# Kernel optimization log

Hardware: AMD Instinct MI355X
Metric: run time of the kernel (lower is better)

The kernel has to match this reference:

```python
import jax, jax.numpy as jnp
import numpy as np

U, I, NG, D, G, B = 100000, 50000, 20000, 64, 20, 16384
H_GE = (D + 2 * D) // 2  # 96, group_encoder hidden

def setup_inputs() -> dict:
    key = jax.random.key(0)
    ks = jax.random.split(key, 24)
    s = 0.1
    return {
        'group_inputs': jax.random.randint(ks[0], (B,), 0, NG),
        'item_inputs': jax.random.randint(ks[1], (B,), 0, I),
        'group_members': jax.random.randint(ks[2], (NG, G), 0, U),
        'eps': jax.random.normal(ks[3], (B, D), dtype=jnp.float32),
        'user_emb': jax.random.normal(ks[4], (U, D), dtype=jnp.float32) * s,
        'item_emb': jax.random.normal(ks[5], (I, D), dtype=jnp.float32) * s,
        # user_encoder: MLP(D, D, 1) -> Linear(D,D), ReLU, Linear(D,D)
        'ue_w1': jax.random.normal(ks[6], (D, D), dtype=jnp.float32) * s,
        'ue_b1': jnp.zeros((D,), jnp.float32),
        'ue_w2': jax.random.normal(ks[7], (D, D), dtype=jnp.float32) * s,
        'ue_b2': jnp.zeros((D,), jnp.float32),
        # group_encoder: MLP(D, 2D, 1) -> Linear(D,96), ReLU, Linear(96,2D)
        'ge_w1': jax.random.normal(ks[8], (D, H_GE), dtype=jnp.float32) * s,
        'ge_b1': jnp.zeros((H_GE,), jnp.float32),
        'ge_w2': jax.random.normal(ks[9], (H_GE, 2 * D), dtype=jnp.float32) * s,
        'ge_b2': jnp.zeros((2 * D,), jnp.float32),
        # attention: Linear(2D,16), ReLU, Linear(16,1)
        'at_w1': jax.random.normal(ks[10], (2 * D, 16), dtype=jnp.float32) * s,
        'at_b1': jnp.zeros((16,), jnp.float32),
        'at_w2': jax.random.normal(ks[11], (16, 1), dtype=jnp.float32) * s,
        'at_b2': jnp.zeros((1,), jnp.float32),
        # predict: Linear(3D,8), ReLU, Linear(8,1)
        'pr_w1': jax.random.normal(ks[12], (3 * D, 8), dtype=jnp.float32) * s,
        'pr_b1': jnp.zeros((8,), jnp.float32),
        'pr_w2': jax.random.normal(ks[13], (8, 1), dtype=jnp.float32) * s,
        'pr_b2': jnp.zeros((1,), jnp.float32),
    }

def reference(group_inputs, item_inputs, group_members, eps,
              user_emb, item_emb,
              ue_w1, ue_b1, ue_w2, ue_b2,
              ge_w1, ge_b1, ge_w2, ge_b2,
              at_w1, at_b1, at_w2, at_b2,
              pr_w1, pr_b1, pr_w2, pr_b2):
    mem_idx = group_members[group_inputs]              # [B, G]
    me = user_emb[mem_idx]                             # [B, G, D] gather
    # user encoder MLP
    enc = jnp.maximum(me @ ue_w1 + ue_b1, 0) @ ue_w2 + ue_b2
    gz = jnp.maximum(jnp.mean(enc, axis=1), 0)         # [B, D]
    gz = jnp.maximum(gz @ ge_w1 + ge_b1, 0) @ ge_w2 + ge_b2  # [B, 2D]
    z_mu, log_sigma = gz[:, :D], gz[:, D:]
    z_sigma = 0.1 + 0.9 * jax.nn.sigmoid(log_sigma)
    ie = item_emb[item_inputs]                          # [B, D]
    gi = jnp.concatenate([me, jnp.broadcast_to(ie[:, None, :], me.shape)], axis=-1)  # [B, G, 2D]
    score = jnp.maximum(gi @ at_w1 + at_b1, 0) @ at_w2 + at_b2  # [B, G, 1]
    w = jax.nn.softmax(score[..., 0], axis=1)           # [B, G]
    g_att = jnp.einsum('bg,bgd->bd', w, me)             # [B, D]
    ge_full = g_att + z_mu + z_sigma * eps              # sample_z with given eps
    ncf = jnp.concatenate([ge_full * ie, ge_full, ie], axis=-1)  # [B, 3D]
    h = jnp.maximum(ncf @ pr_w1 + pr_b1, 0) @ pr_w2 + pr_b2
    return jax.nn.sigmoid(h)                            # [B, 1]
```

## Files before the change

kernel.cpp:

```cpp
#include <hip/hip_runtime.h>
#include <hip/hip_bf16.h>
#include <math.h>

#define G_   20
#define BT   16

typedef __attribute__((ext_vector_type(8))) short bf8;
typedef __attribute__((ext_vector_type(4))) float f4;

#define FMB  0
#define FAT  10
#define FUE2 12
#define FGE1 20
#define FGE2 32
#define FPR  56
#define FTOT 62

__device__ __forceinline__ unsigned cvt2(float x, float y){
    float2 f; f.x = x; f.y = y;
    __hip_bfloat162 h = __float22bfloat162_rn(f);
    return *reinterpret_cast<unsigned*>(&h);
}
__device__ __forceinline__ unsigned short cvt1(float x){
    __hip_bfloat16 h = __float2bfloat16(x);
    return *reinterpret_cast<unsigned short*>(&h);
}
__device__ __forceinline__ bf8 pack8(float4 a, float4 b){
    union { bf8 v; unsigned u[4]; } t;
    t.u[0] = cvt2(a.x, a.y); t.u[1] = cvt2(a.z, a.w);
    t.u[2] = cvt2(b.x, b.y); t.u[3] = cvt2(b.z, b.w);
    return t.v;
}

__global__ __launch_bounds__(256) void vargr_prep(
    const float* __restrict__ ue_w1, const float* __restrict__ ue_w2,
    const float* __restrict__ ge_w1, const float* __restrict__ ge_w2,
    const float* __restrict__ at_w1, const float* __restrict__ pr_w1,
    unsigned short* __restrict__ ws)
{
    int f = blockIdx.x * 256 + threadIdx.x;
    if (f >= FTOT * 64) return;
    int lane = f & 63, grp = f >> 6;
    int col = lane & 15;
    int q8  = (lane >> 4) * 8;
    float v[8];
    if (grp < FAT){
        int g = grp - FMB; int nt = g >> 1; int k0 = (g & 1)*32 + q8; int c = nt*16 + col;
        #pragma unroll
        for (int q = 0; q < 8; ++q)
            v[q] = (c < 64) ? ue_w1[(k0+q)*64 + c] : at_w1[(k0+q)*16 + (c - 64)];
    } else if (grp < FUE2){
        int g = grp - FAT; int k0 = g*32 + q8;
        #pragma unroll
        for (int q = 0; q < 8; ++q) v[q] = at_w1[(64 + k0 + q)*16 + col];
    } else if (grp < FGE1){
        int g = grp - FUE2; int nt = g >> 1; int k0 = (g & 1)*32 + q8;
        #pragma unroll
        for (int q = 0; q < 8; ++q) v[q] = ue_w2[(k0+q)*64 + nt*16 + col];
    } else if (grp < FGE2){
        int g = grp - FGE1; int nt = g >> 1; int k0 = (g & 1)*32 + q8;
        #pragma unroll
        for (int q = 0; q < 8; ++q) v[q] = ge_w1[(k0+q)*96 + nt*16 + col];
    } else if (grp < FPR){
        int g = grp - FGE2; int nt = g / 3; int k0 = (g % 3)*32 + q8;
        #pragma unroll
        for (int q = 0; q < 8; ++q) v[q] = ge_w2[(k0+q)*128 + nt*16 + col];
    } else {
        int g = grp - FPR; int k0 = g*32 + q8;
        #pragma unroll
        for (int q = 0; q < 8; ++q) v[q] = (col < 8) ? pr_w1[(k0+q)*8 + col] : 0.f;
    }
    union { bf8 b; unsigned u[4]; } t;
    t.u[0] = cvt2(v[0], v[1]); t.u[1] = cvt2(v[2], v[3]);
    t.u[2] = cvt2(v[4], v[5]); t.u[3] = cvt2(v[6], v[7]);
    *reinterpret_cast<bf8*>(ws + (size_t)f * 8) = t.b;
}

__global__ __launch_bounds__(256, 2) void vargr_main(
    const int*   __restrict__ group_inputs,
    const int*   __restrict__ item_inputs,
    const int*   __restrict__ group_members,
    const float* __restrict__ eps,
    const float* __restrict__ user_emb,
    const float* __restrict__ item_emb,
    const float* __restrict__ ue_b1, const float* __restrict__ ue_b2,
    const float* __restrict__ ge_b1, const float* __restrict__ ge_b2,
    const float* __restrict__ at_b1, const float* __restrict__ at_w2,
    const float* __restrict__ at_b2, const float* __restrict__ pr_b1,
    const float* __restrict__ pr_w2, const float* __restrict__ pr_b2,
    const unsigned short* __restrict__ ws,
    float* __restrict__ out)
{
    __shared__ unsigned short xAh[BT*136];
    __shared__ unsigned short xBh[BT*136];
    __shared__ float ieb[BT*68];
    __shared__ float gefb[BT*64];
    __shared__ float wsm[BT*G_];
    __shared__ int   sidx[BT*G_];
    __shared__ float x3u[BT*132];

    const int tid = threadIdx.x;
    const int w = tid >> 6, l = tid & 63;
    const int lq = l >> 4, lr = l & 15;
    const int bbase = blockIdx.x * BT;
    const bf8* wsf = (const bf8*)ws;

    bf8 bfr[5][2];
    #pragma unroll
    for (int nt = 0; nt < 5; ++nt)
        #pragma unroll
        for (int kt = 0; kt < 2; ++kt)
            bfr[nt][kt] = wsf[(FMB + nt*2 + kt)*64 + l];
    bf8 abot0 = wsf[(FAT + 0)*64 + l];
    bf8 abot1 = wsf[(FAT + 1)*64 + l];

    float bias1[4];
    #pragma unroll
    for (int nt = 0; nt < 4; ++nt) bias1[nt] = ue_b1[nt*16 + lr];
    const float aw2  = at_w2[lr];
    const float atb2 = at_b2[0];

    {
        int bb = 4*w + lq;
        int item = item_inputs[bbase + bb];
        ((float4*)(ieb + bb*68))[lr] = ((const float4*)(item_emb + (size_t)item*64))[lr];
    }
    if (l < G_){
        #pragma unroll
        for (int i = 0; i < 4; ++i){
            int bb = 4*w + i;
            int gid = group_inputs[bbase + bb];
            sidx[bb*G_ + l] = group_members[gid*G_ + l];
        }
    }
    __syncthreads();

    float4 r0, r1, r2, r3;
    {
        int sx = sidx[(4*w + (lr >> 2))*G_ + 16 + (lr & 3)];
        const float4* p = (const float4*)(user_emb + (size_t)sx*64) + lq*2;
        r0 = p[0]; r1 = p[1]; r2 = p[8]; r3 = p[9];
    }
    float4 c0, c1, c2, c3;
    {
        int sx = sidx[(4*w + 0)*G_ + lr];
        const float4* p = (const float4*)(user_emb + (size_t)sx*64) + lq*2;
        c0 = p[0]; c1 = p[1]; c2 = p[8]; c3 = p[9];
    }

    f4 tvacc = (f4){0.f, 0.f, 0.f, 0.f};
    #pragma unroll
    for (int kt = 0; kt < 2; ++kt){
        const float* ap = ieb + lr*68 + kt*32 + lq*8;
        bf8 a = pack8(*(const float4*)ap, *(const float4*)(ap + 4));
        tvacc = __builtin_amdgcn_mfma_f32_16x16x32_bf16(a, kt ? abot1 : abot0, tvacc, 0, 0, 0);
    }
    const float atb1 = at_b1[lr];
    float tvi[4];
    #pragma unroll
    for (int i = 0; i < 4; ++i)
        tvi[i] = __shfl(tvacc[i], w*16 + lr) + atb1;

    float rem[4];
    {
        bf8 a0 = pack8(r0, r1);
        bf8 a1 = pack8(r2, r3);
        f4 acc[5];
        #pragma unroll
        for (int nt = 0; nt < 5; ++nt) acc[nt] = (f4){0.f, 0.f, 0.f, 0.f};
        #pragma unroll
        for (int nt = 0; nt < 5; ++nt){
            acc[nt] = __builtin_amdgcn_mfma_f32_16x16x32_bf16(a0, bfr[nt][0], acc[nt], 0, 0, 0);
            acc[nt] = __builtin_amdgcn_mfma_f32_16x16x32_bf16(a1, bfr[nt][1], acc[nt], 0, 0, 0);
        }
        #pragma unroll
        for (int nt = 0; nt < 4; ++nt){
            float rs = 0.f;
            #pragma unroll
            for (int rr = 0; rr < 4; ++rr) rs += fmaxf(acc[nt][rr] + bias1[nt], 0.f);
            rem[nt] = rs;
        }
        float tvq = (lq == 0) ? tvi[0] : (lq == 1) ? tvi[1] : (lq == 2) ? tvi[2] : tvi[3];
        float vv[4];
        #pragma unroll
        for (int rr = 0; rr < 4; ++rr) vv[rr] = fmaxf(acc[4][rr] + tvq, 0.f) * aw2;
        #pragma unroll
        for (int rr = 0; rr < 4; ++rr){
            vv[rr] += __shfl_xor(vv[rr], 1, 16);
            vv[rr] += __shfl_xor(vv[rr], 2, 16);
            vv[rr] += __shfl_xor(vv[rr], 4, 16);
            vv[rr] += __shfl_xor(vv[rr], 8, 16);
        }
        if (lr == 0){
            #pragma unroll
            for (int rr = 0; rr < 4; ++rr)
                wsm[(4*w + lq)*G_ + 16 + rr] = vv[rr] + atb2;
        }
    }

    #pragma unroll
    for (int i = 0; i < 4; ++i){
        float4 n0, n1, n2, n3;
        if (i < 3){
            int sx = sidx[(4*w + i + 1)*G_ + lr];
            const float4* p = (const float4*)(user_emb + (size_t)sx*64) + lq*2;
            n0 = p[0]; n1 = p[1]; n2 = p[8]; n3 = p[9];
        }
        const int bb = 4*w + i;
        bf8 a0 = pack8(c0, c1);
        bf8 a1 = pack8(c2, c3);
        f4 acc[5];
        #pragma unroll
        for (int nt = 0; nt < 5; ++nt) acc[nt] = (f4){0.f, 0.f, 0.f, 0.f};
        #pragma unroll
        for (int nt = 0; nt < 5; ++nt){
            acc[nt] = __builtin_amdgcn_mfma_f32_16x16x32_bf16(a0, bfr[nt][0], acc[nt], 0, 0, 0);
            acc[nt] = __builtin_amdgcn_mfma_f32_16x16x32_bf16(a1, bfr[nt][1], acc[nt], 0, 0, 0);
        }
        #pragma unroll
        for (int nt = 0; nt < 4; ++nt){
            float rs = 0.f;
            #pragma unroll
            for (int rr = 0; rr < 4; ++rr) rs += fmaxf(acc[nt][rr] + bias1[nt], 0.f);
            if (lq == i) rs += rem[nt];
            rs += __shfl_xor(rs, 16);
            rs += __shfl_xor(rs, 32);
            if (lq == nt) xAh[bb*136 + nt*16 + lr] = cvt1(rs * (1.f / G_));
        }
        {
            float vv[4];
            #pragma unroll
            for (int rr = 0; rr < 4; ++rr) vv[rr] = fmaxf(acc[4][rr] + tvi[i], 0.f) * aw2;
            #pragma unroll
            for (int rr = 0; rr < 4; ++rr){
                vv[rr] += __shfl_xor(vv[rr], 1, 16);
                vv[rr] += __shfl_xor(vv[rr], 2, 16);
                vv[rr] += __shfl_xor(vv[rr], 4, 16);
                vv[rr] += __shfl_xor(vv[rr], 8, 16);
            }
            if (lr == 0){
                #pragma unroll
                for (int rr = 0; rr < 4; ++rr)
                    wsm[bb*G_ + 4*lq + rr] = vv[rr] + atb2;
            }
        }
        {
            float sval = (l < G_) ? wsm[bb*G_ + l] : -3.0e38f;
            float mx = sval;
            mx = fmaxf(mx, __shfl_xor(mx, 1, 32));
            mx = fmaxf(mx, __shfl_xor(mx, 2, 32));
            mx = fmaxf(mx, __shfl_xor(mx, 4, 32));
            mx = fmaxf(mx, __shfl_xor(mx, 8, 32));
            mx = fmaxf(mx, __shfl_xor(mx, 16, 32));
            float e = (l < G_) ? expf(sval - mx) : 0.f;
            float sm = e;
            sm += __shfl_xor(sm, 1, 32);
            sm += __shfl_xor(sm, 2, 32);
            sm += __shfl_xor(sm, 4, 32);
            sm += __shfl_xor(sm, 8, 32);
            sm += __shfl_xor(sm, 16, 32);
            if (l < G_) wsm[bb*G_ + l] = e / sm;
        }
        {
            float ga = 0.f;
            #pragma unroll
            for (int g = 0; g < G_; ++g)
                ga += wsm[bb*G_ + g] * user_emb[(size_t)sidx[bb*G_ + g]*64 + l];
            gefb[bb*64 + l] = ga;
        }
        c0 = n0; c1 = n1; c2 = n2; c3 = n3;
    }

    float ev[4];
    #pragma unroll
    for (int i = 0; i < 4; ++i)
        ev[i] = eps[(size_t)(bbase + 4*w + i)*64 + l];

    __syncthreads();

    {
        int col = w*16 + lr;
        f4 acc = (f4){0.f, 0.f, 0.f, 0.f};
        #pragma unroll
        for (int kt = 0; kt < 2; ++kt){
            bf8 a = *(const bf8*)(xAh + lr*136 + kt*32 + lq*8);
            acc = __builtin_amdgcn_mfma_f32_16x16x32_bf16(a, wsf[(FUE2 + w*2 + kt)*64 + l], acc, 0, 0, 0);
        }
        float bs = ue_b2[col];
        #pragma unroll
        for (int rr = 0; rr < 4; ++rr)
            xBh[(4*lq + rr)*136 + col] = cvt1(fmaxf(acc[rr] + bs, 0.f));
    }
    __syncthreads();
    for (int t = w; t < 6; t += 4){
        int col = t*16 + lr;
        f4 acc = (f4){0.f, 0.f, 0.f, 0.f};
        #pragma unroll
        for (int kt = 0; kt < 2; ++kt){
            bf8 a = *(const bf8*)(xBh + lr*136 + kt*32 + lq*8);
            acc = __builtin_amdgcn_mfma_f32_16x16x32_bf16(a, wsf[(FGE1 + t*2 + kt)*64 + l], acc, 0, 0, 0);
        }
        float bs = ge_b1[col];
        #pragma unroll
        for (int rr = 0; rr < 4; ++rr)
            xAh[(4*lq + rr)*136 + col] = cvt1(fmaxf(acc[rr] + bs, 0.f));
    }
    __syncthreads();
    for (int t = w; t < 8; t += 4){
        int col = t*16 + lr;
        f4 acc = (f4){0.f, 0.f, 0.f, 0.f};
        #pragma unroll
        for (int kt = 0; kt < 3; ++kt){
            bf8 a = *(const bf8*)(xAh + lr*136 + kt*32 + lq*8);
            acc = __builtin_amdgcn_mfma_f32_16x16x32_bf16(a, wsf[(FGE2 + t*3 + kt)*64 + l], acc, 0, 0, 0);
        }
        float bs = ge_b2[col];
        #pragma unroll
        for (int rr = 0; rr < 4; ++rr)
            x3u[(4*lq + rr)*132 + col] = acc[rr] + bs;
    }
    __syncthreads();

    #pragma unroll
    for (int i = 0; i < 4; ++i){
        int bb = 4*w + i;
        float mu  = x3u[bb*132 + l];
        float sgr = x3u[bb*132 + 64 + l];
        float sg  = 0.1f + 0.9f / (1.f + expf(-sgr));
        gefb[bb*64 + l] += mu + sg * ev[i];
    }
    __syncthreads();
    unsigned short* ncf = (unsigned short*)x3u;
    #pragma unroll
    for (int i = 0; i < 4; ++i){
        int bb = 4*w + i;
        float gef = gefb[bb*64 + l];
        float iev = ieb[bb*68 + l];
        ncf[bb*200 + l]       = cvt1(gef * iev);
        ncf[bb*200 + 64 + l]  = cvt1(gef);
        ncf[bb*200 + 128 + l] = cvt1(iev);
    }
    __syncthreads();
    if (w == 0){
        f4 acc = (f4){0.f, 0.f, 0.f, 0.f};
        #pragma unroll
        for (int kt = 0; kt < 6; ++kt){
            bf8 a = *(const bf8*)(ncf + lr*200 + kt*32 + lq*8);
            acc = __builtin_amdgcn_mfma_f32_16x16x32_bf16(a, wsf[(FPR + kt)*64 + l], acc, 0, 0, 0);
        }
        float pb1 = (lr < 8) ? pr_b1[lr] : 0.f;
        float pw2 = (lr < 8) ? pr_w2[lr] : 0.f;
        float pb2 = pr_b2[0];
        float vv[4];
        #pragma unroll
        for (int rr = 0; rr < 4; ++rr) vv[rr] = fmaxf(acc[rr] + pb1, 0.f) * pw2;
        #pragma unroll
        for (int rr = 0; rr < 4; ++rr){
            vv[rr] += __shfl_xor(vv[rr], 1, 16);
            vv[rr] += __shfl_xor(vv[rr], 2, 16);
            vv[rr] += __shfl_xor(vv[rr], 4, 16);
            vv[rr] += __shfl_xor(vv[rr], 8, 16);
        }
        if (lr == 0){
            #pragma unroll
            for (int rr = 0; rr < 4; ++rr)
                out[bbase + 4*lq + rr] = 1.f / (1.f + expf(-(vv[rr] + pb2)));
        }
    }
}

extern "C" void kernel_launch(void* const* d_in, const int* in_sizes, int n_in,
                              void* d_out, int out_size, void* d_ws, size_t ws_size,
                              hipStream_t stream) {
    const int*   group_inputs  = (const int*)d_in[0];
    const int*   item_inputs   = (const int*)d_in[1];
    const int*   group_members = (const int*)d_in[2];
    const float* eps           = (const float*)d_in[3];
    const float* user_emb      = (const float*)d_in[4];
    const float* item_emb      = (const float*)d_in[5];
    const float* ue_w1 = (const float*)d_in[6];
    const float* ue_b1 = (const float*)d_in[7];
    const float* ue_w2 = (const float*)d_in[8];
    const float* ue_b2 = (const float*)d_in[9];
    const float* ge_w1 = (const float*)d_in[10];
    const float* ge_b1 = (const float*)d_in[11];
    const float* ge_w2 = (const float*)d_in[12];
    const float* ge_b2 = (const float*)d_in[13];
    const float* at_w1 = (const float*)d_in[14];
    const float* at_b1 = (const float*)d_in[15];
    const float* at_w2 = (const float*)d_in[16];
    const float* at_b2 = (const float*)d_in[17];
    const float* pr_w1 = (const float*)d_in[18];
    const float* pr_b1 = (const float*)d_in[19];
    const float* pr_w2 = (const float*)d_in[20];
    const float* pr_b2 = (const float*)d_in[21];
    float* out = (float*)d_out;
    unsigned short* ws = (unsigned short*)d_ws;

    vargr_prep<<<(FTOT*64 + 255)/256, 256, 0, stream>>>(
        ue_w1, ue_w2, ge_w1, ge_w2, at_w1, pr_w1, ws);

    const int nb = in_sizes[0];
    vargr_main<<<nb / BT, 256, 0, stream>>>(
        group_inputs, item_inputs, group_members, eps, user_emb, item_emb,
        ue_b1, ue_b2, ge_b1, ge_b2, at_b1, at_w2, at_b2, pr_b1, pr_w2, pr_b2,
        ws, out);
}
```

Baseline: 41.44 us.

## Run post-gather MLP tail on a single wave, dropping block barriers

After the gather and attention phase, waves 1-3 now exit. Wave 0 alone computes every tile of the user-encoder second layer, both group-encoder layers, the sampling step and the predictor. This removes five __syncthreads between the tail stages and keeps the gef values and all 16 rows of eps in registers. The cost is that tail MFMA work which used to be split across four waves now runs serially on one wave, and register pressure goes up.

```diff
diff --git a/kernel.cpp b/kernel.cpp
--- a/kernel.cpp
+++ b/kernel.cpp
@@ -271,28 +271,30 @@
         c0 = n0; c1 = n1; c2 = n2; c3 = n3;
     }
 
-    float ev[4];
-    #pragma unroll
-    for (int i = 0; i < 4; ++i)
-        ev[i] = eps[(size_t)(bbase + 4*w + i)*64 + l];
-
     __syncthreads();
-
-    {
-        int col = w*16 + lr;
+    if (w != 0) return;
+
+    float ev[16];
+    #pragma unroll
+    for (int bb = 0; bb < BT; ++bb)
+        ev[bb] = eps[(size_t)(bbase + bb)*64 + l];
+
+    #pragma unroll
+    for (int nt = 0; nt < 4; ++nt){
+        int col = nt*16 + lr;
         f4 acc = (f4){0.f, 0.f, 0.f, 0.f};
         #pragma unroll
         for (int kt = 0; kt < 2; ++kt){
             bf8 a = *(const bf8*)(xAh + lr*136 + kt*32 + lq*8);
-            acc = __builtin_amdgcn_mfma_f32_16x16x32_bf16(a, wsf[(FUE2 + w*2 + kt)*64 + l], acc, 0, 0, 0);
+            acc = __builtin_amdgcn_mfma_f32_16x16x32_bf16(a, wsf[(FUE2 + nt*2 + kt)*64 + l], acc, 0, 0, 0);
         }
         float bs = ue_b2[col];
         #pragma unroll
         for (int rr = 0; rr < 4; ++rr)
             xBh[(4*lq + rr)*136 + col] = cvt1(fmaxf(acc[rr] + bs, 0.f));
     }
-    __syncthreads();
-    for (int t = w; t < 6; t += 4){
+    #pragma unroll
+    for (int t = 0; t < 6; ++t){
         int col = t*16 + lr;
         f4 acc = (f4){0.f, 0.f, 0.f, 0.f};
         #pragma unroll
@@ -305,8 +307,8 @@
         for (int rr = 0; rr < 4; ++rr)
             xAh[(4*lq + rr)*136 + col] = cvt1(fmaxf(acc[rr] + bs, 0.f));
     }
-    __syncthreads();
-    for (int t = w; t < 8; t += 4){
+    #pragma unroll
+    for (int t = 0; t < 8; ++t){
         int col = t*16 + lr;
         f4 acc = (f4){0.f, 0.f, 0.f, 0.f};
         #pragma unroll
@@ -319,29 +321,26 @@
         for (int rr = 0; rr < 4; ++rr)
             x3u[(4*lq + rr)*132 + col] = acc[rr] + bs;
     }
-    __syncthreads();
-
-    #pragma unroll
-    for (int i = 0; i < 4; ++i){
-        int bb = 4*w + i;
+
+    float gefv[BT];
+    #pragma unroll
+    for (int bb = 0; bb < BT; ++bb){
         float mu  = x3u[bb*132 + l];
         float sgr = x3u[bb*132 + 64 + l];
         float sg  = 0.1f + 0.9f / (1.f + expf(-sgr));
-        gefb[bb*64 + l] += mu + sg * ev[i];
-    }
-    __syncthreads();
+        gefv[bb] = gefb[bb*64 + l] + mu + sg * ev[bb];
+    }
+    asm volatile("" ::: "memory");
     unsigned short* ncf = (unsigned short*)x3u;
     #pragma unroll
-    for (int i = 0; i < 4; ++i){
-        int bb = 4*w + i;
-        float gef = gefb[bb*64 + l];
+    for (int bb = 0; bb < BT; ++bb){
+        float gef = gefv[bb];
         float iev = ieb[bb*68 + l];
         ncf[bb*200 + l]       = cvt1(gef * iev);
         ncf[bb*200 + 64 + l]  = cvt1(gef);
         ncf[bb*200 + 128 + l] = cvt1(iev);
     }
-    __syncthreads();
-    if (w == 0){
+    {
         f4 acc = (f4){0.f, 0.f, 0.f, 0.f};
         #pragma unroll
         for (int kt = 0; kt < 6; ++kt){
```

Measured after the change: 40.07 us (median of 2 runs). 1.03x faster.
